# Performance work log

Measured on AMD Instinct MI355X. Metric: run time of the kernel, lower is better.

## Reference

```python
import jax, jax.numpy as jnp
import numpy as np

KERNEL_SIZE = (8,)

def setup_inputs() -> dict:
    key = jax.random.key(0)
    k1, = jax.random.split(key, 1)
    inputs = jax.random.normal(k1, (32, 131072, 8), dtype=jnp.float32)
    w = jnp.ones(KERNEL_SIZE, dtype=jnp.float32)  # initializer='ones', non-trainable
    return {"inputs": inputs, "w": w}

def reference(inputs, w):
    # keys[b, n] = sum_c inputs[b, n, c] * w[c]
    keys = jnp.einsum('bnc,c->bn', inputs, w)
    idx = jnp.argsort(keys, axis=-1)                     # [B, N] int
    # batched gather: out[b, i, :] = inputs[b, idx[b, i], :]
    out = jnp.take_along_axis(inputs, idx[:, :, None], axis=1)
    return out
```

## Files before the change

kernel.cpp:

```cpp
#include <hip/hip_runtime.h>


#define NB   32
#define NPB  131072
#define NK   (NB * NPB)
#define TPB  256
#define EPT  16
#define EPB  (TPB * EPT)
#define BPB  (NPB / EPB)
#define NBLK (NB * BPB)
#define BINS 256

typedef unsigned long long u64;
typedef unsigned int u32;

__device__ __forceinline__ u32 fkey(float x) {
    u32 u = __float_as_uint(x);
    return u ^ ((u & 0x80000000u) ? 0xFFFFFFFFu : 0x80000000u);
}

__global__ void keygen(const float* __restrict__ in, const float* __restrict__ w,
                       u64* __restrict__ out)
{
    u32 g = blockIdx.x * TPB + threadIdx.x;
    const float4* p = (const float4*)in + (size_t)g * 2;
    float4 a = p[0], b = p[1];
    float k = __fmul_rn(a.x, w[0]);
    k = __fadd_rn(k, __fmul_rn(a.y, w[1]));
    k = __fadd_rn(k, __fmul_rn(a.z, w[2]));
    k = __fadd_rn(k, __fmul_rn(a.w, w[3]));
    k = __fadd_rn(k, __fmul_rn(b.x, w[4]));
    k = __fadd_rn(k, __fmul_rn(b.y, w[5]));
    k = __fadd_rn(k, __fmul_rn(b.z, w[6]));
    k = __fadd_rn(k, __fmul_rn(b.w, w[7]));
    out[g] = ((u64)fkey(k) << 32) | (u64)(g & (NPB - 1));
}

__global__ void rhist(const u64* __restrict__ src, u32* __restrict__ hist, int shift)
{
    __shared__ u32 h[BINS];
    int t = threadIdx.x;
    h[t] = 0;
    __syncthreads();
    int b = blockIdx.x / BPB, blk = blockIdx.x % BPB;
    size_t base = (size_t)b * NPB + (size_t)blk * EPB;
    int lane = t & 63;
    #pragma unroll
    for (int i = 0; i < EPT; ++i) {
        u64 v = src[base + t + i * TPB];
        u32 d = (u32)(v >> shift) & 255u;
        u64 m = ~0ull;
        #pragma unroll
        for (int k = 0; k < 8; ++k) {
            u64 bk = __ballot((d >> k) & 1u);
            m &= ((d >> k) & 1u) ? bk : ~bk;
        }
        if (lane == __ffsll(m) - 1) atomicAdd(&h[d], (u32)__popcll(m));
    }
    __syncthreads();
    hist[(b * BINS + t) * BPB + blk] = h[t];
}

__global__ void rscan(u32* __restrict__ hist)
{
    int b = blockIdx.x, t = threadIdx.x;
    u32* H = hist + b * BINS * BPB;
    u32 v[32], s = 0;
    #pragma unroll
    for (int k = 0; k < 32; ++k) { v[k] = H[t * 32 + k]; s += v[k]; }
    int lane = t & 63, wid = t >> 6;
    u32 inc = s;
    #pragma unroll
    for (int off = 1; off < 64; off <<= 1) {
        u32 y = __shfl_up(inc, off, 64);
        if (lane >= off) inc += y;
    }
    __shared__ u32 wsum[4];
    if (lane == 63) wsum[wid] = inc;
    __syncthreads();
    u32 wo = 0;
    #pragma unroll
    for (int wI = 0; wI < 4; ++wI) if (wI < wid) wo += wsum[wI];
    u32 run = wo + inc - s;
    #pragma unroll
    for (int k = 0; k < 32; ++k) { u32 c = v[k]; H[t * 32 + k] = run; run += c; }
}

__launch_bounds__(TPB, 4)
__global__ void rscatter(const u64* __restrict__ src, u64* __restrict__ dst,
                         const u32* __restrict__ hist, int shift)
{
    __shared__ u32 s_key[EPB];
    __shared__ u32 s_idx[EPB];
    __shared__ u32 s_wcnt[4][BINS];
    __shared__ u32 s_dbase[BINS];
    __shared__ u32 s_gbase[BINS];
    __shared__ u32 s_wsum[4];
    int t = threadIdx.x, lane = t & 63, wid = t >> 6;
    int b = blockIdx.x / BPB, blk = blockIdx.x % BPB;
    size_t base = (size_t)b * NPB + (size_t)blk * EPB + (size_t)wid * 1024;

    #pragma unroll
    for (int k = 0; k < 4; ++k) ((u32*)s_wcnt)[t + k * TPB] = 0;
    __syncthreads();

    u64 v[EPT];
    u32 rnk[EPT];
    #pragma unroll
    for (int i = 0; i < EPT; ++i) v[i] = src[base + i * 64 + lane];

    #pragma unroll
    for (int i = 0; i < EPT; ++i) {
        u32 d = (u32)(v[i] >> shift) & 255u;
        u64 m = ~0ull;
        #pragma unroll
        for (int k = 0; k < 8; ++k) {
            u64 bk = __ballot((d >> k) & 1u);
            m &= ((d >> k) & 1u) ? bk : ~bk;
        }
        int leader = __ffsll(m) - 1;
        u32 baseCnt = 0;
        if (lane == leader) {
            baseCnt = s_wcnt[wid][d];
            s_wcnt[wid][d] = baseCnt + (u32)__popcll(m);
        }
        baseCnt = __shfl(baseCnt, leader, 64);
        rnk[i] = baseCnt + (u32)__popcll(m & ((1ull << lane) - 1ull));
        __builtin_amdgcn_wave_barrier();
    }
    __syncthreads();

    u32 c0 = s_wcnt[0][t], c1 = s_wcnt[1][t], c2 = s_wcnt[2][t], c3 = s_wcnt[3][t];
    u32 tot = c0 + c1 + c2 + c3;
    s_wcnt[0][t] = 0; s_wcnt[1][t] = c0; s_wcnt[2][t] = c0 + c1; s_wcnt[3][t] = c0 + c1 + c2;
    u32 inc = tot;
    #pragma unroll
    for (int off = 1; off < 64; off <<= 1) {
        u32 y = __shfl_up(inc, off, 64);
        if (lane >= off) inc += y;
    }
    if (lane == 63) s_wsum[wid] = inc;
    __syncthreads();
    u32 wo = 0;
    #pragma unroll
    for (int wI = 0; wI < 4; ++wI) if (wI < wid) wo += s_wsum[wI];
    s_dbase[t] = wo + inc - tot;
    s_gbase[t] = hist[(b * BINS + t) * BPB + blk];
    __syncthreads();

    #pragma unroll
    for (int i = 0; i < EPT; ++i) {
        u32 d = (u32)(v[i] >> shift) & 255u;
        u32 pos = s_dbase[d] + s_wcnt[wid][d] + rnk[i];
        s_key[pos] = (u32)(v[i] >> 32);
        s_idx[pos] = (u32)v[i];
    }
    __syncthreads();

    int kshift = shift - 32;
    #pragma unroll
    for (int i = 0; i < EPT; ++i) {
        int j = i * TPB + t;
        u32 key = s_key[j], idx = s_idx[j];
        u32 d = (key >> kshift) & 255u;
        u32 gpos = s_gbase[d] + (u32)j - s_dbase[d];
        dst[(size_t)b * NPB + gpos] = ((u64)key << 32) | (u64)idx;
    }
}

__global__ void gatherk(const u64* __restrict__ sorted, const float* __restrict__ in,
                        float* __restrict__ out)
{
    u32 g = blockIdx.x * TPB + threadIdx.x;
    u64 v = sorted[g];
    u32 n = (u32)v;
    u32 b = g >> 17;
    const float4* s = (const float4*)in + (((size_t)b << 17) + n) * 2;
    float4 x = s[0], y = s[1];
    float4* d4 = (float4*)out + (size_t)g * 2;
    d4[0] = x; d4[1] = y;
}

extern "C" void kernel_launch(void* const* d_in, const int* in_sizes, int n_in,
                              void* d_out, int out_size, void* d_ws, size_t ws_size,
                              hipStream_t stream)
{
    const float* in = (const float*)d_in[0];
    const float* w  = (const float*)d_in[1];
    float* out = (float*)d_out;

    u64* bufA = (u64*)d_ws;
    u64* bufB = (u64*)d_out;
    u32* hist = (u32*)((char*)d_ws + (size_t)NK * 8);

    keygen<<<NK / TPB, TPB, 0, stream>>>(in, w, bufA);

    u64 *cur = bufA, *alt = bufB;
    for (int p = 0; p < 4; ++p) {
        int shift = 32 + 8 * p;
        rhist<<<NBLK, TPB, 0, stream>>>(cur, hist, shift);
        rscan<<<NB, TPB, 0, stream>>>(hist);
        rscatter<<<NBLK, TPB, 0, stream>>>(cur, alt, hist, shift);
        u64* tmp = cur; cur = alt; alt = tmp;
    }
    gatherk<<<NK / TPB, TPB, 0, stream>>>(cur, in, out);
}
```

Baseline: 265.2 us.

## Fuse keygen into first histogram and gather into last radix scatter

Key generation is folded into the first histogram pass, so the separate keygen kernel and one read of the 8-byte keys are removed. The final scatter now reads the input rows directly and writes them to their sorted positions, which drops the standalone gather kernel and the write/read of the last sorted key buffer. The last pass also remaps block indices so each batch is spread across XCDs (xcd = blockIdx & 7). The cost is scattered 32-byte row writes in the final pass in place of coalesced output writes.

```diff
diff --git a/kernel.cpp b/kernel.cpp
--- a/kernel.cpp
+++ b/kernel.cpp
@@ -19,24 +19,18 @@
     return u ^ ((u & 0x80000000u) ? 0xFFFFFFFFu : 0x80000000u);
 }
 
-__global__ void keygen(const float* __restrict__ in, const float* __restrict__ w,
-                       u64* __restrict__ out)
-{
-    u32 g = blockIdx.x * TPB + threadIdx.x;
-    const float4* p = (const float4*)in + (size_t)g * 2;
-    float4 a = p[0], b = p[1];
-    float k = __fmul_rn(a.x, w[0]);
-    k = __fadd_rn(k, __fmul_rn(a.y, w[1]));
-    k = __fadd_rn(k, __fmul_rn(a.z, w[2]));
-    k = __fadd_rn(k, __fmul_rn(a.w, w[3]));
-    k = __fadd_rn(k, __fmul_rn(b.x, w[4]));
-    k = __fadd_rn(k, __fmul_rn(b.y, w[5]));
-    k = __fadd_rn(k, __fmul_rn(b.z, w[6]));
-    k = __fadd_rn(k, __fmul_rn(b.w, w[7]));
-    out[g] = ((u64)fkey(k) << 32) | (u64)(g & (NPB - 1));
-}
-
-__global__ void rhist(const u64* __restrict__ src, u32* __restrict__ hist, int shift)
+__device__ __forceinline__ u64 matchany(u32 d) {
+    u64 m = ~0ull;
+    #pragma unroll
+    for (int k = 0; k < 8; ++k) {
+        u64 bk = __ballot((d >> k) & 1u);
+        m &= ((d >> k) & 1u) ? bk : ~bk;
+    }
+    return m;
+}
+
+__global__ void khist0(const float* __restrict__ in, const float* __restrict__ w,
+                       u64* __restrict__ outp, u32* __restrict__ hist)
 {
     __shared__ u32 h[BINS];
     int t = threadIdx.x;
@@ -45,16 +39,45 @@
     int b = blockIdx.x / BPB, blk = blockIdx.x % BPB;
     size_t base = (size_t)b * NPB + (size_t)blk * EPB;
     int lane = t & 63;
+    float w0 = w[0], w1 = w[1], w2 = w[2], w3 = w[3];
+    float w4 = w[4], w5 = w[5], w6 = w[6], w7 = w[7];
+    #pragma unroll
+    for (int i = 0; i < EPT; ++i) {
+        size_t row = base + t + i * TPB;
+        const float4* p = (const float4*)in + row * 2;
+        float4 a = p[0], c = p[1];
+        float k = __fmul_rn(a.x, w0);
+        k = __fadd_rn(k, __fmul_rn(a.y, w1));
+        k = __fadd_rn(k, __fmul_rn(a.z, w2));
+        k = __fadd_rn(k, __fmul_rn(a.w, w3));
+        k = __fadd_rn(k, __fmul_rn(c.x, w4));
+        k = __fadd_rn(k, __fmul_rn(c.y, w5));
+        k = __fadd_rn(k, __fmul_rn(c.z, w6));
+        k = __fadd_rn(k, __fmul_rn(c.w, w7));
+        u32 fk = fkey(k);
+        outp[row] = ((u64)fk << 32) | (u64)((u32)row & (NPB - 1));
+        u32 d = fk & 255u;
+        u64 m = matchany(d);
+        if (lane == __ffsll(m) - 1) atomicAdd(&h[d], (u32)__popcll(m));
+    }
+    __syncthreads();
+    hist[(b * BINS + t) * BPB + blk] = h[t];
+}
+
+__global__ void rhist(const u64* __restrict__ src, u32* __restrict__ hist, int shift)
+{
+    __shared__ u32 h[BINS];
+    int t = threadIdx.x;
+    h[t] = 0;
+    __syncthreads();
+    int b = blockIdx.x / BPB, blk = blockIdx.x % BPB;
+    size_t base = (size_t)b * NPB + (size_t)blk * EPB;
+    int lane = t & 63;
     #pragma unroll
     for (int i = 0; i < EPT; ++i) {
         u64 v = src[base + t + i * TPB];
         u32 d = (u32)(v >> shift) & 255u;
-        u64 m = ~0ull;
-        #pragma unroll
-        for (int k = 0; k < 8; ++k) {
-            u64 bk = __ballot((d >> k) & 1u);
-            m &= ((d >> k) & 1u) ? bk : ~bk;
-        }
+        u64 m = matchany(d);
         if (lane == __ffsll(m) - 1) atomicAdd(&h[d], (u32)__popcll(m));
     }
     __syncthreads();
@@ -85,6 +108,58 @@
     #pragma unroll
     for (int k = 0; k < 32; ++k) { u32 c = v[k]; H[t * 32 + k] = run; run += c; }
 }
+
+#define RANK_PERMUTE_BODY(SRC_EXPR)                                             \
+    int t = threadIdx.x, lane = t & 63, wid = t >> 6;                           \
+    size_t base = (size_t)b * NPB + (size_t)blk * EPB + (size_t)wid * 1024;     \
+    _Pragma("unroll")                                                           \
+    for (int k = 0; k < 4; ++k) ((u32*)s_wcnt)[t + k * TPB] = 0;                \
+    __syncthreads();                                                            \
+    u64 v[EPT];                                                                 \
+    u32 rnk[EPT];                                                               \
+    _Pragma("unroll")                                                           \
+    for (int i = 0; i < EPT; ++i) v[i] = (SRC_EXPR);                            \
+    _Pragma("unroll")                                                           \
+    for (int i = 0; i < EPT; ++i) {                                             \
+        u32 d = (u32)(v[i] >> shift) & 255u;                                    \
+        u64 m = matchany(d);                                                    \
+        int leader = __ffsll(m) - 1;                                            \
+        u32 baseCnt = 0;                                                        \
+        if (lane == leader) {                                                   \
+            baseCnt = s_wcnt[wid][d];                                           \
+            s_wcnt[wid][d] = baseCnt + (u32)__popcll(m);                        \
+        }                                                                       \
+        baseCnt = __shfl(baseCnt, leader, 64);                                  \
+        rnk[i] = baseCnt + (u32)__popcll(m & ((1ull << lane) - 1ull));          \
+        __builtin_amdgcn_wave_barrier();                                        \
+    }                                                                           \
+    __syncthreads();                                                            \
+    u32 c0 = s_wcnt[0][t], c1 = s_wcnt[1][t], c2 = s_wcnt[2][t], c3 = s_wcnt[3][t]; \
+    u32 tot = c0 + c1 + c2 + c3;                                                \
+    s_wcnt[0][t] = 0; s_wcnt[1][t] = c0; s_wcnt[2][t] = c0 + c1;                \
+    s_wcnt[3][t] = c0 + c1 + c2;                                                \
+    u32 inc = tot;                                                              \
+    _Pragma("unroll")                                                           \
+    for (int off = 1; off < 64; off <<= 1) {                                    \
+        u32 y = __shfl_up(inc, off, 64);                                        \
+        if (lane >= off) inc += y;                                              \
+    }                                                                           \
+    if (lane == 63) s_wsum[wid] = inc;                                          \
+    __syncthreads();                                                            \
+    u32 wo = 0;                                                                 \
+    _Pragma("unroll")                                                           \
+    for (int wI = 0; wI < 4; ++wI) if (wI < wid) wo += s_wsum[wI];              \
+    s_dbase[t] = wo + inc - tot;                                                \
+    s_gbase[t] = hist[(b * BINS + t) * BPB + blk];                              \
+    __syncthreads();                                                            \
+    _Pragma("unroll")                                                           \
+    for (int i = 0; i < EPT; ++i) {                                             \
+        u32 d = (u32)(v[i] >> shift) & 255u;                                    \
+        u32 pos = s_dbase[d] + s_wcnt[wid][d] + rnk[i];                         \
+        s_key[pos] = (u32)(v[i] >> 32);                                         \
+        s_idx[pos] = (u32)v[i];                                                 \
+    }                                                                           \
+    __syncthreads();
 
 __launch_bounds__(TPB, 4)
 __global__ void rscatter(const u64* __restrict__ src, u64* __restrict__ dst,
@@ -96,66 +171,8 @@
     __shared__ u32 s_dbase[BINS];
     __shared__ u32 s_gbase[BINS];
     __shared__ u32 s_wsum[4];
-    int t = threadIdx.x, lane = t & 63, wid = t >> 6;
     int b = blockIdx.x / BPB, blk = blockIdx.x % BPB;
-    size_t base = (size_t)b * NPB + (size_t)blk * EPB + (size_t)wid * 1024;
-
-    #pragma unroll
-    for (int k = 0; k < 4; ++k) ((u32*)s_wcnt)[t + k * TPB] = 0;
-    __syncthreads();
-
-    u64 v[EPT];
-    u32 rnk[EPT];
-    #pragma unroll
-    for (int i = 0; i < EPT; ++i) v[i] = src[base + i * 64 + lane];
-
-    #pragma unroll
-    for (int i = 0; i < EPT; ++i) {
-        u32 d = (u32)(v[i] >> shift) & 255u;
-        u64 m = ~0ull;
-        #pragma unroll
-        for (int k = 0; k < 8; ++k) {
-            u64 bk = __ballot((d >> k) & 1u);
-            m &= ((d >> k) & 1u) ? bk : ~bk;
-        }
-        int leader = __ffsll(m) - 1;
-        u32 baseCnt = 0;
-        if (lane == leader) {
-            baseCnt = s_wcnt[wid][d];
-            s_wcnt[wid][d] = baseCnt + (u32)__popcll(m);
-        }
-        baseCnt = __shfl(baseCnt, leader, 64);
-        rnk[i] = baseCnt + (u32)__popcll(m & ((1ull << lane) - 1ull));
-        __builtin_amdgcn_wave_barrier();
-    }
-    __syncthreads();
-
-    u32 c0 = s_wcnt[0][t], c1 = s_wcnt[1][t], c2 = s_wcnt[2][t], c3 = s_wcnt[3][t];
-    u32 tot = c0 + c1 + c2 + c3;
-    s_wcnt[0][t] = 0; s_wcnt[1][t] = c0; s_wcnt[2][t] = c0 + c1; s_wcnt[3][t] = c0 + c1 + c2;
-    u32 inc = tot;
-    #pragma unroll
-    for (int off = 1; off < 64; off <<= 1) {
-        u32 y = __shfl_up(inc, off, 64);
-        if (lane >= off) inc += y;
-    }
-    if (lane == 63) s_wsum[wid] = inc;
-    __syncthreads();
-    u32 wo = 0;
-    #pragma unroll
-    for (int wI = 0; wI < 4; ++wI) if (wI < wid) wo += s_wsum[wI];
-    s_dbase[t] = wo + inc - tot;
-    s_gbase[t] = hist[(b * BINS + t) * BPB + blk];
-    __syncthreads();
-
-    #pragma unroll
-    for (int i = 0; i < EPT; ++i) {
-        u32 d = (u32)(v[i] >> shift) & 255u;
-        u32 pos = s_dbase[d] + s_wcnt[wid][d] + rnk[i];
-        s_key[pos] = (u32)(v[i] >> 32);
-        s_idx[pos] = (u32)v[i];
-    }
-    __syncthreads();
+    RANK_PERMUTE_BODY(src[base + i * 64 + lane])
 
     int kshift = shift - 32;
     #pragma unroll
@@ -168,17 +185,35 @@
     }
 }
 
-__global__ void gatherk(const u64* __restrict__ sorted, const float* __restrict__ in,
-                        float* __restrict__ out)
-{
-    u32 g = blockIdx.x * TPB + threadIdx.x;
-    u64 v = sorted[g];
-    u32 n = (u32)v;
-    u32 b = g >> 17;
-    const float4* s = (const float4*)in + (((size_t)b << 17) + n) * 2;
-    float4 x = s[0], y = s[1];
-    float4* d4 = (float4*)out + (size_t)g * 2;
-    d4[0] = x; d4[1] = y;
+__launch_bounds__(TPB, 4)
+__global__ void rscatgat(const u64* __restrict__ src, const float* __restrict__ in,
+                         float* __restrict__ out, const u32* __restrict__ hist)
+{
+    __shared__ u32 s_key[EPB];
+    __shared__ u32 s_idx[EPB];
+    __shared__ u32 s_wcnt[4][BINS];
+    __shared__ u32 s_dbase[BINS];
+    __shared__ u32 s_gbase[BINS];
+    __shared__ u32 s_wsum[4];
+    const int shift = 56;
+    int i0 = blockIdx.x;
+    int xcd = i0 & 7, j0 = i0 >> 3;
+    int b = xcd + 8 * (j0 >> 5), blk = j0 & 31;
+    RANK_PERMUTE_BODY(src[base + i * 64 + lane])
+
+    const float4* inb = (const float4*)in + ((size_t)b << 18);
+    float4* outb = (float4*)out + ((size_t)b << 18);
+    #pragma unroll
+    for (int i = 0; i < EPT; ++i) {
+        int j = i * TPB + t;
+        u32 key = s_key[j], idx = s_idx[j];
+        u32 d = (key >> 24);
+        u32 gpos = s_gbase[d] + (u32)j - s_dbase[d];
+        const float4* s = inb + (size_t)idx * 2;
+        float4 x = s[0], y = s[1];
+        float4* drow = outb + (size_t)gpos * 2;
+        drow[0] = x; drow[1] = y;
+    }
 }
 
 extern "C" void kernel_launch(void* const* d_in, const int* in_sizes, int n_in,
@@ -189,19 +224,23 @@
     const float* w  = (const float*)d_in[1];
     float* out = (float*)d_out;
 
-    u64* bufA = (u64*)d_ws;
-    u64* bufB = (u64*)d_out;
+    u64* A = (u64*)d_ws;
+    u64* B = (u64*)d_out;
     u32* hist = (u32*)((char*)d_ws + (size_t)NK * 8);
 
-    keygen<<<NK / TPB, TPB, 0, stream>>>(in, w, bufA);
-
-    u64 *cur = bufA, *alt = bufB;
-    for (int p = 0; p < 4; ++p) {
-        int shift = 32 + 8 * p;
-        rhist<<<NBLK, TPB, 0, stream>>>(cur, hist, shift);
-        rscan<<<NB, TPB, 0, stream>>>(hist);
-        rscatter<<<NBLK, TPB, 0, stream>>>(cur, alt, hist, shift);
-        u64* tmp = cur; cur = alt; alt = tmp;
-    }
-    gatherk<<<NK / TPB, TPB, 0, stream>>>(cur, in, out);
-}
+    khist0<<<NBLK, TPB, 0, stream>>>(in, w, B, hist);
+    rscan<<<NB, TPB, 0, stream>>>(hist);
+    rscatter<<<NBLK, TPB, 0, stream>>>(B, A, hist, 32);
+
+    rhist<<<NBLK, TPB, 0, stream>>>(A, hist, 40);
+    rscan<<<NB, TPB, 0, stream>>>(hist);
+    rscatter<<<NBLK, TPB, 0, stream>>>(A, B, hist, 40);
+
+    rhist<<<NBLK, TPB, 0, stream>>>(B, hist, 48);
+    rscan<<<NB, TPB, 0, stream>>>(hist);
+    rscatter<<<NBLK, TPB, 0, stream>>>(B, A, hist, 48);
+
+    rhist<<<NBLK, TPB, 0, stream>>>(A, hist, 56);
+    rscan<<<NB, TPB, 0, stream>>>(hist);
+    rscatgat<<<NBLK, TPB, 0, stream>>>(A, in, out, hist);
+}
```

Result: faster. 222.8 us (-16.0%).

## Replace 4-pass LSD radix sort with bucketed MSD partition plus in-LDS bucket sort

Applied to the files above, without the earlier changes.

Builds a 16-bit key-prefix histogram per batch and maps prefixes to about 256 balanced buckets of roughly 512 rows. It then does one global scatter that moves full input rows directly into output bucket positions. Each bucket is finished by a per-block LDS radix sort that recomputes keys and runs only as many 8-bit passes as the key span needs. This replaces four global histogram/scan/scatter passes over 64-bit key-index pairs and the final gather. The cost is global atomics in the prefix histogram, a serial per-thread scan over 65536 bins, and a fixed bucket capacity of 1024 rows, beyond which the rows are silently left unsorted. Stability among equal keys also depends on the order in which rows land inside each bucket.

```diff
diff --git a/kernel.cpp b/kernel.cpp
--- a/kernel.cpp
+++ b/kernel.cpp
@@ -1,42 +1,125 @@
 #include <hip/hip_runtime.h>
 
 
-#define NB   32
-#define NPB  131072
-#define NK   (NB * NPB)
-#define TPB  256
-#define EPT  16
-#define EPB  (TPB * EPT)
-#define BPB  (NPB / EPB)
-#define NBLK (NB * BPB)
-#define BINS 256
+#define NB    32
+#define NPB   131072
+#define NK    (NB * NPB)
+#define TPB   256
+#define EPT   16
+#define EPB   (TPB * EPT)
+#define BPB   (NPB / EPB)
+#define NBLK  (NB * BPB)
+#define BINS  256
+#define PBINS 65536
+#define BCAP  1024
+#define BEPT  4
 
 typedef unsigned long long u64;
 typedef unsigned int u32;
+typedef unsigned short u16;
+typedef unsigned char u8;
 
 __device__ __forceinline__ u32 fkey(float x) {
     u32 u = __float_as_uint(x);
     return u ^ ((u & 0x80000000u) ? 0xFFFFFFFFu : 0x80000000u);
 }
 
-__global__ void keygen(const float* __restrict__ in, const float* __restrict__ w,
-                       u64* __restrict__ out)
-{
-    u32 g = blockIdx.x * TPB + threadIdx.x;
-    const float4* p = (const float4*)in + (size_t)g * 2;
-    float4 a = p[0], b = p[1];
-    float k = __fmul_rn(a.x, w[0]);
-    k = __fadd_rn(k, __fmul_rn(a.y, w[1]));
-    k = __fadd_rn(k, __fmul_rn(a.z, w[2]));
-    k = __fadd_rn(k, __fmul_rn(a.w, w[3]));
-    k = __fadd_rn(k, __fmul_rn(b.x, w[4]));
-    k = __fadd_rn(k, __fmul_rn(b.y, w[5]));
-    k = __fadd_rn(k, __fmul_rn(b.z, w[6]));
-    k = __fadd_rn(k, __fmul_rn(b.w, w[7]));
-    out[g] = ((u64)fkey(k) << 32) | (u64)(g & (NPB - 1));
-}
-
-__global__ void rhist(const u64* __restrict__ src, u32* __restrict__ hist, int shift)
+__device__ __forceinline__ float seqdot(float4 a, float4 c,
+                                        float w0, float w1, float w2, float w3,
+                                        float w4, float w5, float w6, float w7) {
+    float k = __fmul_rn(a.x, w0);
+    k = __fadd_rn(k, __fmul_rn(a.y, w1));
+    k = __fadd_rn(k, __fmul_rn(a.z, w2));
+    k = __fadd_rn(k, __fmul_rn(a.w, w3));
+    k = __fadd_rn(k, __fmul_rn(c.x, w4));
+    k = __fadd_rn(k, __fmul_rn(c.y, w5));
+    k = __fadd_rn(k, __fmul_rn(c.z, w6));
+    k = __fadd_rn(k, __fmul_rn(c.w, w7));
+    return k;
+}
+
+__device__ __forceinline__ u64 matchany(u32 d) {
+    u64 m = ~0ull;
+    #pragma unroll
+    for (int k = 0; k < 8; ++k) {
+        u64 bk = __ballot((d >> k) & 1u);
+        m &= ((d >> k) & 1u) ? bk : ~bk;
+    }
+    return m;
+}
+
+__global__ void zeroH(u32* __restrict__ h16)
+{
+    h16[blockIdx.x * TPB + threadIdx.x] = 0;
+}
+
+__global__ void khistP(const float* __restrict__ in, const float* __restrict__ w,
+                       u32* __restrict__ keys, u32* __restrict__ h16)
+{
+    int t = threadIdx.x;
+    int b = blockIdx.x / BPB, blk = blockIdx.x % BPB;
+    size_t base = (size_t)b * NPB + (size_t)blk * EPB;
+    u32* h = h16 + (size_t)b * PBINS;
+    float w0 = w[0], w1 = w[1], w2 = w[2], w3 = w[3];
+    float w4 = w[4], w5 = w[5], w6 = w[6], w7 = w[7];
+    #pragma unroll
+    for (int i = 0; i < EPT; ++i) {
+        size_t row = base + t + i * TPB;
+        const float4* p = (const float4*)in + row * 2;
+        float4 a = p[0], c = p[1];
+        u32 fk = fkey(seqdot(a, c, w0, w1, w2, w3, w4, w5, w6, w7));
+        keys[row] = fk;
+        atomicAdd(&h[fk >> 16], 1u);
+    }
+}
+
+__global__ void mapscan(const u32* __restrict__ h16, u8* __restrict__ map8,
+                        u32* __restrict__ bstart)
+{
+    __shared__ u32 wsum[4];
+    __shared__ u32 prevb[TPB];
+    int b = blockIdx.x, t = threadIdx.x, lane = t & 63, wid = t >> 6;
+    const u32* H = h16 + (size_t)b * PBINS;
+    u8* M = map8 + (size_t)b * PBINS;
+    u32* BS = bstart + b * 257;
+
+    u32 s = 0;
+    for (int k = 0; k < 256; ++k) s += H[t * 256 + k];
+    u32 inc = s;
+    #pragma unroll
+    for (int off = 1; off < 64; off <<= 1) {
+        u32 y = __shfl_up(inc, off, 64);
+        if (lane >= off) inc += y;
+    }
+    if (lane == 63) wsum[wid] = inc;
+    __syncthreads();
+    u32 wo = 0;
+    #pragma unroll
+    for (int wI = 0; wI < 4; ++wI) if (wI < wid) wo += wsum[wI];
+    u32 texcl = wo + inc - s;
+
+    u32 lastcnt = H[t * 256 + 255];
+    u32 lastc = texcl + s - lastcnt;
+    u32 lb = lastc >> 9; if (lb > 255u) lb = 255u;
+    prevb[t] = lb;
+    __syncthreads();
+
+    int lastbkt = (t == 0) ? -1 : (int)prevb[t - 1];
+    u32 c = texcl;
+    for (int k = 0; k < 256; ++k) {
+        int p = t * 256 + k;
+        u32 cntp = H[p];
+        u32 bkt = c >> 9; if (bkt > 255u) bkt = 255u;
+        M[p] = (u8)bkt;
+        for (int j = lastbkt + 1; j <= (int)bkt; ++j) BS[j] = c;
+        lastbkt = (int)bkt;
+        c += cntp;
+    }
+    if (t == TPB - 1) BS[256] = NPB;
+}
+
+__global__ void khist0v(const u32* __restrict__ keys, const u8* __restrict__ map8,
+                        u32* __restrict__ hist)
 {
     __shared__ u32 h[BINS];
     int t = threadIdx.x;
@@ -44,17 +127,13 @@
     __syncthreads();
     int b = blockIdx.x / BPB, blk = blockIdx.x % BPB;
     size_t base = (size_t)b * NPB + (size_t)blk * EPB;
+    const u8* M = map8 + (size_t)b * PBINS;
     int lane = t & 63;
     #pragma unroll
     for (int i = 0; i < EPT; ++i) {
-        u64 v = src[base + t + i * TPB];
-        u32 d = (u32)(v >> shift) & 255u;
-        u64 m = ~0ull;
-        #pragma unroll
-        for (int k = 0; k < 8; ++k) {
-            u64 bk = __ballot((d >> k) & 1u);
-            m &= ((d >> k) & 1u) ? bk : ~bk;
-        }
+        u32 k = keys[base + t + i * TPB];
+        u32 d = M[k >> 16];
+        u64 m = matchany(d);
         if (lane == __ffsll(m) - 1) atomicAdd(&h[d], (u32)__popcll(m));
     }
     __syncthreads();
@@ -87,37 +166,37 @@
 }
 
 __launch_bounds__(TPB, 4)
-__global__ void rscatter(const u64* __restrict__ src, u64* __restrict__ dst,
-                         const u32* __restrict__ hist, int shift)
-{
-    __shared__ u32 s_key[EPB];
-    __shared__ u32 s_idx[EPB];
+__global__ void scatA(const float* __restrict__ in, const u32* __restrict__ keys,
+                      const u8* __restrict__ map8, float* __restrict__ out,
+                      const u32* __restrict__ hist)
+{
+    __shared__ u32 s_pack[EPB];
     __shared__ u32 s_wcnt[4][BINS];
     __shared__ u32 s_dbase[BINS];
     __shared__ u32 s_gbase[BINS];
     __shared__ u32 s_wsum[4];
     int t = threadIdx.x, lane = t & 63, wid = t >> 6;
     int b = blockIdx.x / BPB, blk = blockIdx.x % BPB;
-    size_t base = (size_t)b * NPB + (size_t)blk * EPB + (size_t)wid * 1024;
+    const float4* inw = (const float4*)in + ((size_t)b * NPB + (size_t)blk * EPB) * 2;
+    const u32* kw = keys + (size_t)b * NPB + (size_t)blk * EPB;
+    const u8* M = map8 + (size_t)b * PBINS;
 
     #pragma unroll
     for (int k = 0; k < 4; ++k) ((u32*)s_wcnt)[t + k * TPB] = 0;
     __syncthreads();
 
-    u64 v[EPT];
+    u32 dgt[EPT];
     u32 rnk[EPT];
     #pragma unroll
-    for (int i = 0; i < EPT; ++i) v[i] = src[base + i * 64 + lane];
-
-    #pragma unroll
-    for (int i = 0; i < EPT; ++i) {
-        u32 d = (u32)(v[i] >> shift) & 255u;
-        u64 m = ~0ull;
-        #pragma unroll
-        for (int k = 0; k < 8; ++k) {
-            u64 bk = __ballot((d >> k) & 1u);
-            m &= ((d >> k) & 1u) ? bk : ~bk;
-        }
+    for (int i = 0; i < EPT; ++i) {
+        u32 k = kw[wid * 1024 + i * 64 + lane];
+        dgt[i] = M[k >> 16];
+    }
+
+    #pragma unroll
+    for (int i = 0; i < EPT; ++i) {
+        u32 d = dgt[i];
+        u64 m = matchany(d);
         int leader = __ffsll(m) - 1;
         u32 baseCnt = 0;
         if (lane == leader) {
@@ -150,35 +229,152 @@
 
     #pragma unroll
     for (int i = 0; i < EPT; ++i) {
-        u32 d = (u32)(v[i] >> shift) & 255u;
+        u32 d = dgt[i];
         u32 pos = s_dbase[d] + s_wcnt[wid][d] + rnk[i];
-        s_key[pos] = (u32)(v[i] >> 32);
-        s_idx[pos] = (u32)v[i];
-    }
-    __syncthreads();
-
-    int kshift = shift - 32;
+        u32 srcpos = (u32)(wid * 1024 + i * 64 + lane);
+        s_pack[pos] = (d << 12) | srcpos;
+    }
+    __syncthreads();
+
+    float4* outb = (float4*)out + ((size_t)b << 18);
     #pragma unroll
     for (int i = 0; i < EPT; ++i) {
         int j = i * TPB + t;
-        u32 key = s_key[j], idx = s_idx[j];
-        u32 d = (key >> kshift) & 255u;
+        u32 pack = s_pack[j];
+        u32 d = pack >> 12;
+        u32 sp = pack & 4095u;
         u32 gpos = s_gbase[d] + (u32)j - s_dbase[d];
-        dst[(size_t)b * NPB + gpos] = ((u64)key << 32) | (u64)idx;
-    }
-}
-
-__global__ void gatherk(const u64* __restrict__ sorted, const float* __restrict__ in,
-                        float* __restrict__ out)
-{
-    u32 g = blockIdx.x * TPB + threadIdx.x;
-    u64 v = sorted[g];
-    u32 n = (u32)v;
-    u32 b = g >> 17;
-    const float4* s = (const float4*)in + (((size_t)b << 17) + n) * 2;
-    float4 x = s[0], y = s[1];
-    float4* d4 = (float4*)out + (size_t)g * 2;
-    d4[0] = x; d4[1] = y;
+        float4 x = inw[2 * sp], y = inw[2 * sp + 1];
+        float4* dr = outb + (size_t)gpos * 2;
+        dr[0] = x; dr[1] = y;
+    }
+}
+
+__launch_bounds__(TPB, 3)
+__global__ void sortB(float* __restrict__ data, const float* __restrict__ w,
+                      const u32* __restrict__ bstart)
+{
+    __shared__ float4 s_rows[BCAP * 2];
+    __shared__ u32 s_keyA[BCAP];
+    __shared__ u32 s_keyB[BCAP];
+    __shared__ u16 s_posA[BCAP];
+    __shared__ u16 s_posB[BCAP];
+    __shared__ u32 s_wcnt[4][BINS];
+    __shared__ u32 s_dbase[BINS];
+    __shared__ u32 s_wsum[4];
+    __shared__ u32 s_mn[4], s_mx[4];
+
+    int b = blockIdx.x >> 8;
+    int bk = blockIdx.x & 255;
+    u32 start = bstart[b * 257 + bk];
+    u32 end   = bstart[b * 257 + bk + 1];
+    u32 cnt = end - start;
+    if (cnt == 0) return;
+    if (cnt > BCAP) cnt = BCAP;
+
+    int t = threadIdx.x, lane = t & 63, wid = t >> 6;
+    float4* base4 = (float4*)data + ((size_t)b * NPB + start) * 2;
+
+    for (u32 j = t; j < cnt * 2; j += TPB) s_rows[j] = base4[j];
+    __syncthreads();
+
+    float w0 = w[0], w1 = w[1], w2 = w[2], w3 = w[3];
+    float w4 = w[4], w5 = w[5], w6 = w[6], w7 = w[7];
+    u32 kmin = 0xFFFFFFFFu, kmax = 0;
+    for (u32 j = t; j < cnt; j += TPB) {
+        float4 a = s_rows[2 * j], c = s_rows[2 * j + 1];
+        u32 fk = fkey(seqdot(a, c, w0, w1, w2, w3, w4, w5, w6, w7));
+        s_keyA[j] = fk;
+        kmin = (fk < kmin) ? fk : kmin;
+        kmax = (fk > kmax) ? fk : kmax;
+    }
+    #pragma unroll
+    for (int off = 1; off < 64; off <<= 1) {
+        u32 a = __shfl_xor(kmin, off, 64);
+        u32 z = __shfl_xor(kmax, off, 64);
+        kmin = (a < kmin) ? a : kmin;
+        kmax = (z > kmax) ? z : kmax;
+    }
+    if (lane == 0) { s_mn[wid] = kmin; s_mx[wid] = kmax; }
+    __syncthreads();
+    kmin = s_mn[0]; kmax = s_mx[0];
+    #pragma unroll
+    for (int wI = 1; wI < 4; ++wI) {
+        kmin = (s_mn[wI] < kmin) ? s_mn[wI] : kmin;
+        kmax = (s_mx[wI] > kmax) ? s_mx[wI] : kmax;
+    }
+    u32 span = kmax - kmin;
+    if (span == 0) return;
+
+    for (u32 j = t; j < cnt; j += TPB) { s_keyA[j] -= kmin; s_posA[j] = (u16)j; }
+    for (u32 j = cnt + t; j < BCAP; j += TPB) { s_keyA[j] = 0xFFFFFFFFu; s_posA[j] = (u16)j; }
+    int npasses = (39 - __clz(span)) >> 3;
+
+    u32* keyS = s_keyA; u32* keyD = s_keyB;
+    u16* posS = s_posA; u16* posD = s_posB;
+
+    for (int p = 0; p < npasses; ++p) {
+        int sh = 8 * p;
+        #pragma unroll
+        for (int k = 0; k < 4; ++k) ((u32*)s_wcnt)[t + k * TPB] = 0;
+        __syncthreads();
+
+        u32 kk[BEPT], rr[BEPT], dd[BEPT];
+        #pragma unroll
+        for (int i = 0; i < BEPT; ++i) {
+            int e = wid * 256 + i * 64 + lane;
+            kk[i] = keyS[e];
+            u32 dg = (kk[i] >> sh) & 255u;
+            dd[i] = dg;
+            u64 m = matchany(dg);
+            int leader = __ffsll(m) - 1;
+            u32 bc = 0;
+            if (lane == leader) {
+                bc = s_wcnt[wid][dg];
+                s_wcnt[wid][dg] = bc + (u32)__popcll(m);
+            }
+            bc = __shfl(bc, leader, 64);
+            rr[i] = bc + (u32)__popcll(m & ((1ull << lane) - 1ull));
+            __builtin_amdgcn_wave_barrier();
+        }
+        __syncthreads();
+
+        u32 c0 = s_wcnt[0][t], c1 = s_wcnt[1][t], c2 = s_wcnt[2][t], c3 = s_wcnt[3][t];
+        u32 tot = c0 + c1 + c2 + c3;
+        s_wcnt[0][t] = 0; s_wcnt[1][t] = c0; s_wcnt[2][t] = c0 + c1; s_wcnt[3][t] = c0 + c1 + c2;
+        u32 inc = tot;
+        #pragma unroll
+        for (int off = 1; off < 64; off <<= 1) {
+            u32 y = __shfl_up(inc, off, 64);
+            if (lane >= off) inc += y;
+        }
+        if (lane == 63) s_wsum[wid] = inc;
+        __syncthreads();
+        u32 wo = 0;
+        #pragma unroll
+        for (int wI = 0; wI < 4; ++wI) if (wI < wid) wo += s_wsum[wI];
+        s_dbase[t] = wo + inc - tot;
+        __syncthreads();
+
+        #pragma unroll
+        for (int i = 0; i < BEPT; ++i) {
+            int e = wid * 256 + i * 64 + lane;
+            u32 dg = dd[i];
+            u32 np = s_dbase[dg] + s_wcnt[wid][dg] + rr[i];
+            keyD[np] = kk[i];
+            posD[np] = posS[e];
+        }
+        __syncthreads();
+
+        u32* tk = keyS; keyS = keyD; keyD = tk;
+        u16* tp = posS; posS = posD; posD = tp;
+    }
+
+    for (u32 j = t; j < cnt; j += TPB) {
+        u32 sp = posS[j];
+        float4 x = s_rows[2 * sp], y = s_rows[2 * sp + 1];
+        base4[2 * j] = x; base4[2 * j + 1] = y;
+    }
 }
 
 extern "C" void kernel_launch(void* const* d_in, const int* in_sizes, int n_in,
@@ -189,19 +385,19 @@
     const float* w  = (const float*)d_in[1];
     float* out = (float*)d_out;
 
-    u64* bufA = (u64*)d_ws;
-    u64* bufB = (u64*)d_out;
-    u32* hist = (u32*)((char*)d_ws + (size_t)NK * 8);
-
-    keygen<<<NK / TPB, TPB, 0, stream>>>(in, w, bufA);
-
-    u64 *cur = bufA, *alt = bufB;
-    for (int p = 0; p < 4; ++p) {
-        int shift = 32 + 8 * p;
-        rhist<<<NBLK, TPB, 0, stream>>>(cur, hist, shift);
-        rscan<<<NB, TPB, 0, stream>>>(hist);
-        rscatter<<<NBLK, TPB, 0, stream>>>(cur, alt, hist, shift);
-        u64* tmp = cur; cur = alt; alt = tmp;
-    }
-    gatherk<<<NK / TPB, TPB, 0, stream>>>(cur, in, out);
-}
+    char* wsb = (char*)d_ws;
+    u32* keys   = (u32*)wsb;
+    u32* h16    = (u32*)(wsb + (size_t)NK * 4);
+    u8*  map8   = (u8*) (wsb + (size_t)NK * 4 + (size_t)NB * PBINS * 4);
+    u32* hist   = (u32*)(wsb + (size_t)NK * 4 + (size_t)NB * PBINS * 5);
+    u32* bstart = (u32*)(wsb + (size_t)NK * 4 + (size_t)NB * PBINS * 5
+                             + (size_t)NB * BINS * BPB * 4);
+
+    zeroH<<<NB * PBINS / TPB, TPB, 0, stream>>>(h16);
+    khistP<<<NBLK, TPB, 0, stream>>>(in, w, keys, h16);
+    mapscan<<<NB, TPB, 0, stream>>>(h16, map8, bstart);
+    khist0v<<<NBLK, TPB, 0, stream>>>(keys, map8, hist);
+    rscan<<<NB, TPB, 0, stream>>>(hist);
+    scatA<<<NBLK, TPB, 0, stream>>>(in, keys, map8, out, hist);
+    sortB<<<NB * BINS, TPB, 0, stream>>>(out, w, bstart);
+}
```

After: 446.1 us. +68.2%, slower.
